# Kernel tuning notes

Hardware: AMD Instinct MI355X
Metric: run time of the kernel (lower is better)

## Reference

```python
import jax, jax.numpy as jnp
import numpy as np

KS = 5
NF = 64
B, H, W = 2, 160, 160


def _conv1x1(x, w, b):
    # x: (B,Ci,H,W), w: (Co,Ci)
    return jnp.einsum('oi,bihw->bohw', w, x) + b[None, :, None, None]


def _conv2x2(x, w, b, dil):
    # x: (B,1,Hp,Wp), w: (64,1,2,2); VALID conv with dilation dil
    y = jax.lax.conv_general_dilated(x, w, (1, 1), 'VALID',
                                     rhs_dilation=(dil, dil),
                                     dimension_numbers=('NCHW', 'OIHW', 'NCHW'))
    return y + b[None, :, None, None]


def _conv_s(x, w, b):
    # conv1 module, mode 's': gather taps (0,0),(1,1),(1,2),(2,1) of each 3x3 patch,
    # then (1,4) conv == linear combo of 4 shifted images.
    h = x.shape[2] - 2
    wd = x.shape[3] - 2
    x0 = x[:, 0]
    taps = jnp.stack([x0[:, 0:h, 0:wd],
                      x0[:, 1:h + 1, 1:wd + 1],
                      x0[:, 1:h + 1, 2:wd + 2],
                      x0[:, 2:h + 2, 1:wd + 1]], axis=1)  # (B,4,h,wd)
    return jnp.einsum('ok,bkhw->bohw', w.reshape(NF, 4), taps) + b[None, :, None, None]


def _construct(c, dense_ps):
    # relu then dense 1x1-conv chain with channel concat, final 1x1 -> 4 channels
    x = jax.nn.relu(c)
    for (wt, bs) in dense_ps[:-1]:
        feat = jax.nn.relu(_conv1x1(x, wt, bs))
        x = jnp.concatenate([x, feat], axis=1)
    wt, bs = dense_ps[-1]
    return _conv1x1(x, wt, bs)


def _ag(x, sigx, sigy, theta, sigr):
    # x: (B,ks,ks,HW); params: (B,HW). Per-pixel anisotropic bilateral kernel.
    ks = x.shape[1]
    r = jnp.arange(ks, dtype=x.dtype) - ks // 2
    sq = (r[:, None] ** 2 + r[None, :] ** 2)[None, :, :, None]  # (1,ks,ks,1)
    sx = sigx[:, None, None, :]
    sy = sigy[:, None, None, :]
    th = theta[:, None, None, :]
    sr = sigr[:, None, None, :]
    spatial = jnp.exp(-sq / (2.0 * sr ** 2))
    disx = jnp.abs(x[:, ks // 2:ks // 2 + 1] - x)       # center row
    disy = jnp.abs(x[:, :, ks // 2:ks // 2 + 1] - x)    # center col
    a = sx * disx
    bb = sy * disy
    color = jnp.exp(-0.5 * (a ** 2 - 2.0 * th * a * bb + bb ** 2))
    kern = spatial * color
    kern = kern / jnp.sum(kern, axis=(1, 2), keepdims=True)
    return jnp.sum(kern * x, axis=(1, 2))  # (B,HW)


def _forward(x_in, conv1x_w, conv1x_b, conv1c_w, conv1c_b, conv1cs_w, conv1cs_b,
             w2, b2, w3, b3, w4, b4, w5, b5, w6, b6):
    dense_ps = [(w2, b2), (w3, b3), (w4, b4), (w5, b5), (w6, b6)]

    def fk(x, mod):
        if mod == 's':
            c = _conv_s(x, conv1cs_w, conv1cs_b)
        elif mod == 'c':
            c = _conv2x2(x, conv1c_w, conv1c_b, 2)
        else:
            c = _conv2x2(x, conv1x_w, conv1x_b, 1)
        return _construct(c, dense_ps)

    def mode_ens(x, p, mod):
        pad = lambda z: jnp.pad(z, ((0, 0), (0, 0), (0, p), (0, p)), mode='reflect')
        r0 = fk(pad(x), mod)
        r2 = jnp.rot90(fk(pad(jnp.rot90(x, 2, (2, 3))), mod), 2, (2, 3))
        r1 = jnp.rot90(fk(pad(jnp.rot90(x, 1, (2, 3))), mod), 3, (2, 3))
        r3 = jnp.rot90(fk(pad(jnp.rot90(x, 3, (2, 3))), mod), 1, (2, 3))
        return (r0 + r2) / 2.0, (r1 + r3) / 2.0

    e1x, e2x = mode_ens(x_in, 1, 'x')
    e1s, e2s = mode_ens(x_in, 2, 's')
    e1c, e2c = mode_ens(x_in, 2, 'c')
    par = (e1x + e2x + e1s + e2s + e1c + e2c) / 6.0  # (B,4,H,W)

    b, c, h, w = x_in.shape
    sigx = jnp.clip(jax.nn.sigmoid(par[:, 0]).reshape(b, -1) + 1e-6, 0.0, 1.0)
    sigy = jnp.clip(jax.nn.sigmoid(par[:, 1]).reshape(b, -1) + 1e-6, 0.0, 1.0)
    theta = jnp.clip(jnp.tanh(par[:, 2]).reshape(b, -1), -1.0, 1.0)
    sigr = jnp.clip(jnp.tanh(par[:, 3]).reshape(b, -1) + 1e-6, -1.0, 1.0)

    ph = KS // 2
    xt = jnp.pad(x_in, ((0, 0), (0, 0), (ph, ph), (ph, ph)))  # zero pad
    # unfold -> (B, KS, KS, H*W)
    patches = jnp.stack([jnp.stack([xt[:, 0, i:i + h, j:j + w].reshape(b, -1)
                                    for j in range(KS)], axis=1)
                         for i in range(KS)], axis=1)
    outs = _ag(patches, sigx * 20.0, sigy * 20.0, theta, sigr * 10.0 + 10.0).reshape(b, c, h, w)
    return outs, sigx, sigy, theta, sigr


def setup_inputs() -> dict:
    key = jax.random.key(0)
    k = jax.random.split(key, 10)
    def kn(kk, shape, fan_in):
        return jax.random.normal(kk, shape, jnp.float32) * np.float32(np.sqrt(2.0 / fan_in))
    zb = lambda n: jnp.zeros((n,), jnp.float32)
    return {
        'x_in': jax.random.normal(k[0], (B, 1, H, W), jnp.float32),
        'conv1x_w': kn(k[1], (NF, 1, 2, 2), 4), 'conv1x_b': zb(NF),
        'conv1c_w': kn(k[2], (NF, 1, 2, 2), 4), 'conv1c_b': zb(NF),
        'conv1cs_w': kn(k[3], (NF, 1, 1, 4), 4), 'conv1cs_b': zb(NF),
        'w2': kn(k[4], (NF, NF), NF), 'b2': zb(NF),
        'w3': kn(k[5], (NF, 2 * NF), 2 * NF), 'b3': zb(NF),
        'w4': kn(k[6], (NF, 3 * NF), 3 * NF), 'b4': zb(NF),
        'w5': kn(k[7], (NF, 4 * NF), 4 * NF), 'b5': zb(NF),
        'w6': kn(k[8], (4, 5 * NF), 5 * NF), 'b6': zb(4),
    }


def reference(x_in, conv1x_w, conv1x_b, conv1c_w, conv1c_b, conv1cs_w, conv1cs_b,
              w2, b2, w3, b3, w4, b4, w5, b5, w6, b6):
    return _forward(x_in, conv1x_w, conv1x_b, conv1c_w, conv1c_b, conv1cs_w, conv1cs_b,
                    w2, b2, w3, b3, w4, b4, w5, b5, w6, b6)
```

## Files before the change

### kernel.cpp

```cpp
#include <hip/hip_runtime.h>
#include <hip/hip_bf16.h>
#include <math.h>
#include <string.h>


#define NN   160
#define NPIX 25600

typedef __attribute__((ext_vector_type(4))) float float4v;
typedef __attribute__((ext_vector_type(8))) unsigned short ushort8;
typedef __attribute__((ext_vector_type(2))) unsigned int uint2v;
typedef __attribute__((ext_vector_type(4))) unsigned int uint4v;
typedef __attribute__((ext_vector_type(8))) __bf16 bf16x8;

__device__ __forceinline__ int refp(int a) { return (a <= NN - 1) ? a : (2 * (NN - 1) - a); }

__device__ __forceinline__ unsigned short f2b(float f) {
    unsigned int x = __float_as_uint(f);
    return (unsigned short)((x + 0x7FFFu + ((x >> 16) & 1u)) >> 16);
}
__device__ __forceinline__ unsigned int pk2(float lo, float hi) {
    float2 f; f.x = lo; f.y = hi;
    __hip_bfloat162 h = __float22bfloat162_rn(f);
    unsigned int u;
    memcpy(&u, &h, 4);
    return u;
}

__global__ __launch_bounds__(256) void bnet_wconv_kernel(
    const float* __restrict__ w2, const float* __restrict__ w3,
    const float* __restrict__ w4, const float* __restrict__ w5,
    const float* __restrict__ w6, unsigned short* __restrict__ wb)
{
    const int t = blockIdx.x * 256 + threadIdx.x;
    if (t < 4096)       wb[t] = f2b(w2[t]);
    else if (t < 12288) wb[t] = f2b(w3[t - 4096]);
    else if (t < 24576) wb[t] = f2b(w4[t - 12288]);
    else if (t < 40960) wb[t] = f2b(w5[t - 24576]);
    else {
        const int i = t - 40960;
        wb[t] = (i < 4 * 320) ? f2b(w6[i]) : (unsigned short)0;
    }
}

template <int NCH>
__device__ __forceinline__ void dense_layer(const ushort8 (&A)[NCH], float4v biasv,
                                            unsigned short* Xs, int w, int lo16, int lq) {
    const int K = NCH * 32;
#pragma unroll
    for (int pp = 0; pp < 2; ++pp) {
        const int px0 = (pp * 2) * 16 + lo16;
        const int px1 = (pp * 2 + 1) * 16 + lo16;
        float4v acc0 = biasv, acc1 = biasv;
#pragma unroll
        for (int s = 0; s < NCH; ++s) {
            const int c8 = s * 4 + lq;
            const bf16x8 bf0 = __builtin_bit_cast(bf16x8, *(const ushort8*)&Xs[c8 * 512 + px0 * 8]);
            const bf16x8 bf1 = __builtin_bit_cast(bf16x8, *(const ushort8*)&Xs[c8 * 512 + px1 * 8]);
            const bf16x8 af  = __builtin_bit_cast(bf16x8, A[s]);
            acc0 = __builtin_amdgcn_mfma_f32_16x16x32_bf16(af, bf0, acc0, 0, 0, 0);
            acc1 = __builtin_amdgcn_mfma_f32_16x16x32_bf16(af, bf1, acc1, 0, 0, 0);
        }
        const int cb = K + w * 16 + lq * 4;
        uint2v o0, o1;
        o0[0] = pk2(fmaxf(acc0[0], 0.0f), fmaxf(acc0[1], 0.0f));
        o0[1] = pk2(fmaxf(acc0[2], 0.0f), fmaxf(acc0[3], 0.0f));
        o1[0] = pk2(fmaxf(acc1[0], 0.0f), fmaxf(acc1[1], 0.0f));
        o1[1] = pk2(fmaxf(acc1[2], 0.0f), fmaxf(acc1[3], 0.0f));
        *(uint2v*)&Xs[(cb >> 3) * 512 + px0 * 8 + (cb & 7)] = o0;
        *(uint2v*)&Xs[(cb >> 3) * 512 + px1 * 8 + (cb & 7)] = o1;
    }
    __syncthreads();
}

__global__ __launch_bounds__(256, 4) void bnet_mlp_kernel(
    const float* __restrict__ x,
    const float* __restrict__ wx, const float* __restrict__ bx,
    const float* __restrict__ wcs, const float* __restrict__ bcs,
    const float* __restrict__ wc, const float* __restrict__ bc,
    const unsigned short* __restrict__ wb,
    const float* __restrict__ b2, const float* __restrict__ b3,
    const float* __restrict__ b4, const float* __restrict__ b5,
    float* __restrict__ par)
{
    __shared__ unsigned short Xs[20480];
    float* red = (float*)Xs;

    const int t = threadIdx.x;
    const int lane = t & 63;
    const int lo16 = lane & 15;
    const int lq = lane >> 4;
    const int w = __builtin_amdgcn_readfirstlane(t >> 6);

    const int bid = blockIdx.x;
    const int tile = bid % 400;
    const int b = (bid / 400) & 1;
    const int mode = (bid / 800) % 3;
    const int k = bid / 2400;

    const float* xb = x + b * NPIX;
    const float* w1 = (mode == 0) ? wx : (mode == 1) ? wcs : wc;
    const float* b1 = (mode == 0) ? bx : (mode == 1) ? bcs : bc;
    int DY[4], DX[4];
    if (mode == 0)      { DY[0]=0; DY[1]=0; DY[2]=1; DY[3]=1;  DX[0]=0; DX[1]=1; DX[2]=0; DX[3]=1; }
    else if (mode == 1) { DY[0]=0; DY[1]=1; DY[2]=1; DY[3]=2;  DX[0]=0; DX[1]=1; DX[2]=2; DX[3]=1; }
    else                { DY[0]=0; DY[1]=0; DY[2]=2; DY[3]=2;  DX[0]=0; DX[1]=2; DX[2]=0; DX[3]=2; }

    const int arow = w * 16 + lo16;
    ushort8 a2[2], a3[4], a4[6], a5[8], a6[3];
#pragma unroll
    for (int s = 0; s < 2; ++s) a2[s] = *(const ushort8*)&wb[arow * 64 + s * 32 + lq * 8];
#pragma unroll
    for (int s = 0; s < 4; ++s) a3[s] = *(const ushort8*)&wb[4096 + arow * 128 + s * 32 + lq * 8];
#pragma unroll
    for (int s = 0; s < 6; ++s) a4[s] = *(const ushort8*)&wb[12288 + arow * 192 + s * 32 + lq * 8];
#pragma unroll
    for (int s = 0; s < 8; ++s) a5[s] = *(const ushort8*)&wb[24576 + arow * 256 + s * 32 + lq * 8];
#pragma unroll
    for (int c = 0; c < 3; ++c) {
        const int ch = (3 * w + c) * 32;
        if (ch < 320) {
            a6[c] = *(const ushort8*)&wb[40960 + lo16 * 320 + ch + lq * 8];
        } else {
            ushort8 z = {0, 0, 0, 0, 0, 0, 0, 0};
            a6[c] = z;
        }
    }
    const float4v b2v = *(const float4v*)&b2[w * 16 + lq * 4];
    const float4v b3v = *(const float4v*)&b3[w * 16 + lq * 4];
    const float4v b4v = *(const float4v*)&b4[w * 16 + lq * 4];
    const float4v b5v = *(const float4v*)&b5[w * 16 + lq * 4];

    const int pix = tile * 64 + lane;
    const int pi = pix / NN;
    const int pj = pix - pi * NN;

    float s4[4];
#pragma unroll
    for (int tt = 0; tt < 4; ++tt) {
        const int dy = DY[tt], dx = DX[tt];
        int r, c;
        if (k == 0)      { r = refp(pi + dy); c = refp(pj + dx); }
        else if (k == 1) { r = refp(pi + dx); c = (pj >= dy) ? (pj - dy) : (dy - pj); }
        else if (k == 2) { r = (pi >= dy) ? (pi - dy) : (dy - pi);
                           c = (pj >= dx) ? (pj - dx) : (dx - pj); }
        else             { r = (pi >= dx) ? (pi - dx) : (dx - pi); c = refp(pj + dy); }
        s4[tt] = xb[r * NN + c];
    }
    float co[16];
#pragma unroll
    for (int oo = 0; oo < 16; ++oo) {
        const int o = w * 16 + oo;
        float cacc = b1[o];
#pragma unroll
        for (int tt = 0; tt < 4; ++tt) cacc = fmaf(w1[o * 4 + tt], s4[tt], cacc);
        co[oo] = fmaxf(cacc, 0.0f);
    }
    uint4v pka, pkb;
#pragma unroll
    for (int q = 0; q < 4; ++q) {
        pka[q] = pk2(co[2 * q], co[2 * q + 1]);
        pkb[q] = pk2(co[8 + 2 * q], co[9 + 2 * q]);
    }
    *(uint4v*)&Xs[(w * 2) * 512 + lane * 8]     = pka;
    *(uint4v*)&Xs[(w * 2 + 1) * 512 + lane * 8] = pkb;
    __syncthreads();

    dense_layer<2>(a2, b2v, Xs, w, lo16, lq);
    dense_layer<4>(a3, b3v, Xs, w, lo16, lq);
    dense_layer<6>(a4, b4v, Xs, w, lo16, lq);
    dense_layer<8>(a5, b5v, Xs, w, lo16, lq);

    float4v acc6[4];
#pragma unroll
    for (int pt = 0; pt < 4; ++pt) { float4v z = {0.f, 0.f, 0.f, 0.f}; acc6[pt] = z; }
#pragma unroll
    for (int pt = 0; pt < 4; ++pt) {
        const int px = pt * 16 + lo16;
#pragma unroll
        for (int c = 0; c < 3; ++c) {
            int chb = (3 * w + c) * 32;
            chb = (chb < 288) ? chb : 288;
            const int c8 = (chb >> 3) + lq;
            const bf16x8 bf = __builtin_bit_cast(
                bf16x8, *(const ushort8*)&Xs[c8 * 512 + px * 8]);
            const bf16x8 af = __builtin_bit_cast(bf16x8, a6[c]);
            acc6[pt] = __builtin_amdgcn_mfma_f32_16x16x32_bf16(af, bf, acc6[pt], 0, 0, 0);
        }
    }
    __syncthreads();

    if (lq == 0) {
#pragma unroll
        for (int pt = 0; pt < 4; ++pt)
            *(float4v*)&red[(((w * 4) + pt) * 16 + lo16) * 4] = acc6[pt];
    }
    __syncthreads();
    if (w == 0) {
        float4v sv;
#pragma unroll
        for (int r = 0; r < 4; ++r)
            sv[r] = red[(((0 * 4) + lq) * 16 + lo16) * 4 + r]
                  + red[(((1 * 4) + lq) * 16 + lo16) * 4 + r]
                  + red[(((2 * 4) + lq) * 16 + lo16) * 4 + r]
                  + red[(((3 * 4) + lq) * 16 + lo16) * 4 + r];
        const int pixg = tile * 64 + lq * 16 + lo16;
#pragma unroll
        for (int r = 0; r < 4; ++r)
            atomicAdd(&par[(r * 2 + b) * NPIX + pixg], sv[r]);
    }
}

__global__ __launch_bounds__(256) void bnet_bilateral_kernel(
    const float* __restrict__ x, const float* __restrict__ b6,
    float* __restrict__ out)
{
    const int tid = blockIdx.x * 256 + threadIdx.x;
    const int b = tid / NPIX;
    const int pix = tid - b * NPIX;
    const int pi = pix / NN;
    const int pj = pix - pi * NN;

    float* par = out + 2 * NPIX;
    const float inv12 = 1.0f / 12.0f;
    const float p0 = par[(0 + b) * NPIX + pix] * inv12 + b6[0];
    const float p1 = par[(2 + b) * NPIX + pix] * inv12 + b6[1];
    const float p2 = par[(4 + b) * NPIX + pix] * inv12 + b6[2];
    const float p3 = par[(6 + b) * NPIX + pix] * inv12 + b6[3];

    float sigx = 1.0f / (1.0f + __expf(-p0)) + 1e-6f;
    sigx = fminf(fmaxf(sigx, 0.0f), 1.0f);
    float sigy = 1.0f / (1.0f + __expf(-p1)) + 1e-6f;
    sigy = fminf(fmaxf(sigy, 0.0f), 1.0f);
    float t2 = __expf(2.0f * fminf(fmaxf(p2, -15.0f), 15.0f));
    float th = (t2 - 1.0f) / (t2 + 1.0f);
    th = fminf(fmaxf(th, -1.0f), 1.0f);
    float t3 = __expf(2.0f * fminf(fmaxf(p3, -15.0f), 15.0f));
    float sigr = (t3 - 1.0f) / (t3 + 1.0f) + 1e-6f;
    sigr = fminf(fmaxf(sigr, -1.0f), 1.0f);

    par[(0 + b) * NPIX + pix] = sigx;
    par[(2 + b) * NPIX + pix] = sigy;
    par[(4 + b) * NPIX + pix] = th;
    par[(6 + b) * NPIX + pix] = sigr;

    const float sx = sigx * 20.0f;
    const float sy = sigy * 20.0f;
    const float sr = sigr * 10.0f + 10.0f;

    const float* xb = x + b * NPIX;
    float patch[5][5];
#pragma unroll
    for (int ky = 0; ky < 5; ++ky) {
#pragma unroll
        for (int kx = 0; kx < 5; ++kx) {
            const int r = pi + ky - 2, c = pj + kx - 2;
            patch[ky][kx] = (r >= 0 && r < NN && c >= 0 && c < NN) ? xb[r * NN + c] : 0.0f;
        }
    }

    const float inv2sr2 = 1.0f / (2.0f * sr * sr);
    float num = 0.0f, den = 0.0f;
#pragma unroll
    for (int ky = 0; ky < 5; ++ky) {
#pragma unroll
        for (int kx = 0; kx < 5; ++kx) {
            const float v = patch[ky][kx];
            const float dxv = fabsf(patch[2][kx] - v);
            const float dyv = fabsf(patch[ky][2] - v);
            const float a = sx * dxv;
            const float bb = sy * dyv;
            const float sq = (float)((ky - 2) * (ky - 2) + (kx - 2) * (kx - 2));
            const float kern = __expf(-sq * inv2sr2 - 0.5f * (a * a - 2.0f * th * a * bb + bb * bb));
            den += kern;
            num = fmaf(kern, v, num);
        }
    }
    out[tid] = num / den;
}

extern "C" void kernel_launch(void* const* d_in, const int* in_sizes, int n_in,
                              void* d_out, int out_size, void* d_ws, size_t ws_size,
                              hipStream_t stream) {
    const float* x   = (const float*)d_in[0];
    const float* wx  = (const float*)d_in[1];
    const float* bx  = (const float*)d_in[2];
    const float* wc  = (const float*)d_in[3];
    const float* bc  = (const float*)d_in[4];
    const float* wcs = (const float*)d_in[5];
    const float* bcs = (const float*)d_in[6];
    const float* w2  = (const float*)d_in[7];
    const float* b2  = (const float*)d_in[8];
    const float* w3  = (const float*)d_in[9];
    const float* b3  = (const float*)d_in[10];
    const float* w4  = (const float*)d_in[11];
    const float* b4  = (const float*)d_in[12];
    const float* w5  = (const float*)d_in[13];
    const float* b5  = (const float*)d_in[14];
    const float* w6  = (const float*)d_in[15];
    const float* b6  = (const float*)d_in[16];
    float* out = (float*)d_out;
    unsigned short* wb = (unsigned short*)d_ws;

    (void)hipMemsetAsync(out + 2 * NPIX, 0, 8 * NPIX * sizeof(float), stream);

    hipLaunchKernelGGL(bnet_wconv_kernel, dim3(180), dim3(256), 0, stream,
                       w2, w3, w4, w5, w6, wb);

    hipLaunchKernelGGL(bnet_mlp_kernel, dim3(9600), dim3(256), 0, stream,
                       x, wx, bx, wcs, bcs, wc, bc,
                       wb, b2, b3, b4, b5,
                       out + 2 * NPIX);

    hipLaunchKernelGGL(bnet_bilateral_kernel, dim3(200), dim3(256), 0, stream,
                       x, b6, out);
}
```

Baseline: 198.9 us.

## Make MLP kernel persistent and convert weights to bf16 in-kernel

The MLP kernel becomes a persistent grid of 768 blocks, each looping over 12-13 (tile, batch, mode, k) work items. Each block loads its MFMA weight fragments into registers once, converting fp32 to bf16 on the fly. This removes the separate weight-conversion kernel launch and the per-block weight reload that 9600 short-lived blocks paid. In exchange, occupancy is capped at 3 blocks per CU and an extra barrier is added per iteration.

```diff
diff --git a/kernel.cpp b/kernel.cpp
--- a/kernel.cpp
+++ b/kernel.cpp
@@ -15,10 +15,6 @@
 
 __device__ __forceinline__ int refp(int a) { return (a <= NN - 1) ? a : (2 * (NN - 1) - a); }
 
-__device__ __forceinline__ unsigned short f2b(float f) {
-    unsigned int x = __float_as_uint(f);
-    return (unsigned short)((x + 0x7FFFu + ((x >> 16) & 1u)) >> 16);
-}
 __device__ __forceinline__ unsigned int pk2(float lo, float hi) {
     float2 f; f.x = lo; f.y = hi;
     __hip_bfloat162 h = __float22bfloat162_rn(f);
@@ -26,21 +22,13 @@
     memcpy(&u, &h, 4);
     return u;
 }
-
-__global__ __launch_bounds__(256) void bnet_wconv_kernel(
-    const float* __restrict__ w2, const float* __restrict__ w3,
-    const float* __restrict__ w4, const float* __restrict__ w5,
-    const float* __restrict__ w6, unsigned short* __restrict__ wb)
-{
-    const int t = blockIdx.x * 256 + threadIdx.x;
-    if (t < 4096)       wb[t] = f2b(w2[t]);
-    else if (t < 12288) wb[t] = f2b(w3[t - 4096]);
-    else if (t < 24576) wb[t] = f2b(w4[t - 12288]);
-    else if (t < 40960) wb[t] = f2b(w5[t - 24576]);
-    else {
-        const int i = t - 40960;
-        wb[t] = (i < 4 * 320) ? f2b(w6[i]) : (unsigned short)0;
-    }
+__device__ __forceinline__ ushort8 cvt8(const float* __restrict__ p) {
+    const float4v f0 = *(const float4v*)p;
+    const float4v f1 = *(const float4v*)(p + 4);
+    uint4v u;
+    u[0] = pk2(f0[0], f0[1]); u[1] = pk2(f0[2], f0[3]);
+    u[2] = pk2(f1[0], f1[1]); u[3] = pk2(f1[2], f1[3]);
+    return __builtin_bit_cast(ushort8, u);
 }
 
 template <int NCH>
@@ -73,14 +61,16 @@
     __syncthreads();
 }
 
-__global__ __launch_bounds__(256, 4) void bnet_mlp_kernel(
+__global__ __launch_bounds__(256, 3) void bnet_mlp_kernel(
     const float* __restrict__ x,
     const float* __restrict__ wx, const float* __restrict__ bx,
     const float* __restrict__ wcs, const float* __restrict__ bcs,
     const float* __restrict__ wc, const float* __restrict__ bc,
-    const unsigned short* __restrict__ wb,
-    const float* __restrict__ b2, const float* __restrict__ b3,
-    const float* __restrict__ b4, const float* __restrict__ b5,
+    const float* __restrict__ w2, const float* __restrict__ b2,
+    const float* __restrict__ w3, const float* __restrict__ b3,
+    const float* __restrict__ w4, const float* __restrict__ b4,
+    const float* __restrict__ w5, const float* __restrict__ b5,
+    const float* __restrict__ w6,
     float* __restrict__ par)
 {
     __shared__ unsigned short Xs[20480];
@@ -92,35 +82,21 @@
     const int lq = lane >> 4;
     const int w = __builtin_amdgcn_readfirstlane(t >> 6);
 
-    const int bid = blockIdx.x;
-    const int tile = bid % 400;
-    const int b = (bid / 400) & 1;
-    const int mode = (bid / 800) % 3;
-    const int k = bid / 2400;
-
-    const float* xb = x + b * NPIX;
-    const float* w1 = (mode == 0) ? wx : (mode == 1) ? wcs : wc;
-    const float* b1 = (mode == 0) ? bx : (mode == 1) ? bcs : bc;
-    int DY[4], DX[4];
-    if (mode == 0)      { DY[0]=0; DY[1]=0; DY[2]=1; DY[3]=1;  DX[0]=0; DX[1]=1; DX[2]=0; DX[3]=1; }
-    else if (mode == 1) { DY[0]=0; DY[1]=1; DY[2]=1; DY[3]=2;  DX[0]=0; DX[1]=1; DX[2]=2; DX[3]=1; }
-    else                { DY[0]=0; DY[1]=0; DY[2]=2; DY[3]=2;  DX[0]=0; DX[1]=2; DX[2]=0; DX[3]=2; }
-
     const int arow = w * 16 + lo16;
     ushort8 a2[2], a3[4], a4[6], a5[8], a6[3];
 #pragma unroll
-    for (int s = 0; s < 2; ++s) a2[s] = *(const ushort8*)&wb[arow * 64 + s * 32 + lq * 8];
-#pragma unroll
-    for (int s = 0; s < 4; ++s) a3[s] = *(const ushort8*)&wb[4096 + arow * 128 + s * 32 + lq * 8];
-#pragma unroll
-    for (int s = 0; s < 6; ++s) a4[s] = *(const ushort8*)&wb[12288 + arow * 192 + s * 32 + lq * 8];
-#pragma unroll
-    for (int s = 0; s < 8; ++s) a5[s] = *(const ushort8*)&wb[24576 + arow * 256 + s * 32 + lq * 8];
+    for (int s = 0; s < 2; ++s) a2[s] = cvt8(&w2[arow * 64 + s * 32 + lq * 8]);
+#pragma unroll
+    for (int s = 0; s < 4; ++s) a3[s] = cvt8(&w3[arow * 128 + s * 32 + lq * 8]);
+#pragma unroll
+    for (int s = 0; s < 6; ++s) a4[s] = cvt8(&w4[arow * 192 + s * 32 + lq * 8]);
+#pragma unroll
+    for (int s = 0; s < 8; ++s) a5[s] = cvt8(&w5[arow * 256 + s * 32 + lq * 8]);
 #pragma unroll
     for (int c = 0; c < 3; ++c) {
         const int ch = (3 * w + c) * 32;
-        if (ch < 320) {
-            a6[c] = *(const ushort8*)&wb[40960 + lo16 * 320 + ch + lq * 8];
+        if (ch < 320 && lo16 < 4) {
+            a6[c] = cvt8(&w6[lo16 * 320 + ch + lq * 8]);
         } else {
             ushort8 z = {0, 0, 0, 0, 0, 0, 0, 0};
             a6[c] = z;
@@ -131,83 +107,107 @@
     const float4v b4v = *(const float4v*)&b4[w * 16 + lq * 4];
     const float4v b5v = *(const float4v*)&b5[w * 16 + lq * 4];
 
-    const int pix = tile * 64 + lane;
-    const int pi = pix / NN;
-    const int pj = pix - pi * NN;
-
-    float s4[4];
-#pragma unroll
-    for (int tt = 0; tt < 4; ++tt) {
-        const int dy = DY[tt], dx = DX[tt];
-        int r, c;
-        if (k == 0)      { r = refp(pi + dy); c = refp(pj + dx); }
-        else if (k == 1) { r = refp(pi + dx); c = (pj >= dy) ? (pj - dy) : (dy - pj); }
-        else if (k == 2) { r = (pi >= dy) ? (pi - dy) : (dy - pi);
-                           c = (pj >= dx) ? (pj - dx) : (dx - pj); }
-        else             { r = (pi >= dx) ? (pi - dx) : (dx - pi); c = refp(pj + dy); }
-        s4[tt] = xb[r * NN + c];
-    }
-    float co[16];
-#pragma unroll
-    for (int oo = 0; oo < 16; ++oo) {
-        const int o = w * 16 + oo;
-        float cacc = b1[o];
-#pragma unroll
-        for (int tt = 0; tt < 4; ++tt) cacc = fmaf(w1[o * 4 + tt], s4[tt], cacc);
-        co[oo] = fmaxf(cacc, 0.0f);
-    }
-    uint4v pka, pkb;
-#pragma unroll
-    for (int q = 0; q < 4; ++q) {
-        pka[q] = pk2(co[2 * q], co[2 * q + 1]);
-        pkb[q] = pk2(co[8 + 2 * q], co[9 + 2 * q]);
-    }
-    *(uint4v*)&Xs[(w * 2) * 512 + lane * 8]     = pka;
-    *(uint4v*)&Xs[(w * 2 + 1) * 512 + lane * 8] = pkb;
-    __syncthreads();
-
-    dense_layer<2>(a2, b2v, Xs, w, lo16, lq);
-    dense_layer<4>(a3, b3v, Xs, w, lo16, lq);
-    dense_layer<6>(a4, b4v, Xs, w, lo16, lq);
-    dense_layer<8>(a5, b5v, Xs, w, lo16, lq);
-
-    float4v acc6[4];
-#pragma unroll
-    for (int pt = 0; pt < 4; ++pt) { float4v z = {0.f, 0.f, 0.f, 0.f}; acc6[pt] = z; }
-#pragma unroll
-    for (int pt = 0; pt < 4; ++pt) {
-        const int px = pt * 16 + lo16;
-#pragma unroll
-        for (int c = 0; c < 3; ++c) {
-            int chb = (3 * w + c) * 32;
-            chb = (chb < 288) ? chb : 288;
-            const int c8 = (chb >> 3) + lq;
-            const bf16x8 bf = __builtin_bit_cast(
-                bf16x8, *(const ushort8*)&Xs[c8 * 512 + px * 8]);
-            const bf16x8 af = __builtin_bit_cast(bf16x8, a6[c]);
-            acc6[pt] = __builtin_amdgcn_mfma_f32_16x16x32_bf16(af, bf, acc6[pt], 0, 0, 0);
-        }
-    }
-    __syncthreads();
-
-    if (lq == 0) {
-#pragma unroll
-        for (int pt = 0; pt < 4; ++pt)
-            *(float4v*)&red[(((w * 4) + pt) * 16 + lo16) * 4] = acc6[pt];
-    }
-    __syncthreads();
-    if (w == 0) {
-        float4v sv;
-#pragma unroll
-        for (int r = 0; r < 4; ++r)
-            sv[r] = red[(((0 * 4) + lq) * 16 + lo16) * 4 + r]
-                  + red[(((1 * 4) + lq) * 16 + lo16) * 4 + r]
-                  + red[(((2 * 4) + lq) * 16 + lo16) * 4 + r]
-                  + red[(((3 * 4) + lq) * 16 + lo16) * 4 + r];
-        const int pixg = tile * 64 + lq * 16 + lo16;
-#pragma unroll
-        for (int r = 0; r < 4; ++r)
-            atomicAdd(&par[(r * 2 + b) * NPIX + pixg], sv[r]);
+    const int bid = blockIdx.x;
+    const int nit = 12 + (bid < 384 ? 1 : 0);
+    const int g0  = (bid < 384) ? bid * 13 : bid * 12 + 384;
+
+    for (int it = 0; it < nit; ++it) {
+        const int g = g0 + it;
+        const int v = g % 12;
+        const int tb = g / 12;
+        const int tile = tb >> 1;
+        const int b = tb & 1;
+        const int mode = v >> 2;
+        const int k = v & 3;
+
+        const float* xb = x + b * NPIX;
+        const float* w1 = (mode == 0) ? wx : (mode == 1) ? wcs : wc;
+        const float* b1 = (mode == 0) ? bx : (mode == 1) ? bcs : bc;
+        int DY[4], DX[4];
+        if (mode == 0)      { DY[0]=0; DY[1]=0; DY[2]=1; DY[3]=1;  DX[0]=0; DX[1]=1; DX[2]=0; DX[3]=1; }
+        else if (mode == 1) { DY[0]=0; DY[1]=1; DY[2]=1; DY[3]=2;  DX[0]=0; DX[1]=1; DX[2]=2; DX[3]=1; }
+        else                { DY[0]=0; DY[1]=0; DY[2]=2; DY[3]=2;  DX[0]=0; DX[1]=2; DX[2]=0; DX[3]=2; }
+
+        const int pix = tile * 64 + lane;
+        const int pi = pix / NN;
+        const int pj = pix - pi * NN;
+
+        __syncthreads();
+
+        float s4[4];
+#pragma unroll
+        for (int tt = 0; tt < 4; ++tt) {
+            const int dy = DY[tt], dx = DX[tt];
+            int r, c;
+            if (k == 0)      { r = refp(pi + dy); c = refp(pj + dx); }
+            else if (k == 1) { r = refp(pi + dx); c = (pj >= dy) ? (pj - dy) : (dy - pj); }
+            else if (k == 2) { r = (pi >= dy) ? (pi - dy) : (dy - pi);
+                               c = (pj >= dx) ? (pj - dx) : (dx - pj); }
+            else             { r = (pi >= dx) ? (pi - dx) : (dx - pi); c = refp(pj + dy); }
+            s4[tt] = xb[r * NN + c];
+        }
+        float co[16];
+#pragma unroll
+        for (int oo = 0; oo < 16; ++oo) {
+            const int o = w * 16 + oo;
+            float cacc = b1[o];
+#pragma unroll
+            for (int tt = 0; tt < 4; ++tt) cacc = fmaf(w1[o * 4 + tt], s4[tt], cacc);
+            co[oo] = fmaxf(cacc, 0.0f);
+        }
+        uint4v pka, pkb;
+#pragma unroll
+        for (int q = 0; q < 4; ++q) {
+            pka[q] = pk2(co[2 * q], co[2 * q + 1]);
+            pkb[q] = pk2(co[8 + 2 * q], co[9 + 2 * q]);
+        }
+        *(uint4v*)&Xs[(w * 2) * 512 + lane * 8]     = pka;
+        *(uint4v*)&Xs[(w * 2 + 1) * 512 + lane * 8] = pkb;
+        __syncthreads();
+
+        dense_layer<2>(a2, b2v, Xs, w, lo16, lq);
+        dense_layer<4>(a3, b3v, Xs, w, lo16, lq);
+        dense_layer<6>(a4, b4v, Xs, w, lo16, lq);
+        dense_layer<8>(a5, b5v, Xs, w, lo16, lq);
+
+        float4v acc6[4];
+#pragma unroll
+        for (int pt = 0; pt < 4; ++pt) { float4v z = {0.f, 0.f, 0.f, 0.f}; acc6[pt] = z; }
+#pragma unroll
+        for (int pt = 0; pt < 4; ++pt) {
+            const int px = pt * 16 + lo16;
+#pragma unroll
+            for (int c = 0; c < 3; ++c) {
+                int chb = (3 * w + c) * 32;
+                chb = (chb < 288) ? chb : 288;
+                const int c8 = (chb >> 3) + lq;
+                const bf16x8 bf = __builtin_bit_cast(
+                    bf16x8, *(const ushort8*)&Xs[c8 * 512 + px * 8]);
+                const bf16x8 af = __builtin_bit_cast(bf16x8, a6[c]);
+                acc6[pt] = __builtin_amdgcn_mfma_f32_16x16x32_bf16(af, bf, acc6[pt], 0, 0, 0);
+            }
+        }
+        __syncthreads();
+
+        if (lq == 0) {
+#pragma unroll
+            for (int pt = 0; pt < 4; ++pt)
+                *(float4v*)&red[(((w * 4) + pt) * 16 + lo16) * 4] = acc6[pt];
+        }
+        __syncthreads();
+        if (w == 0) {
+            float4v sv;
+#pragma unroll
+            for (int r = 0; r < 4; ++r)
+                sv[r] = red[(((0 * 4) + lq) * 16 + lo16) * 4 + r]
+                      + red[(((1 * 4) + lq) * 16 + lo16) * 4 + r]
+                      + red[(((2 * 4) + lq) * 16 + lo16) * 4 + r]
+                      + red[(((3 * 4) + lq) * 16 + lo16) * 4 + r];
+            const int pixg = tile * 64 + lq * 16 + lo16;
+#pragma unroll
+            for (int r = 0; r < 4; ++r)
+                atomicAdd(&par[(r * 2 + b) * NPIX + pixg], sv[r]);
+        }
     }
 }
 
@@ -300,16 +300,12 @@
     const float* w6  = (const float*)d_in[15];
     const float* b6  = (const float*)d_in[16];
     float* out = (float*)d_out;
-    unsigned short* wb = (unsigned short*)d_ws;
 
     (void)hipMemsetAsync(out + 2 * NPIX, 0, 8 * NPIX * sizeof(float), stream);
 
-    hipLaunchKernelGGL(bnet_wconv_kernel, dim3(180), dim3(256), 0, stream,
-                       w2, w3, w4, w5, w6, wb);
-
-    hipLaunchKernelGGL(bnet_mlp_kernel, dim3(9600), dim3(256), 0, stream,
+    hipLaunchKernelGGL(bnet_mlp_kernel, dim3(768), dim3(256), 0, stream,
                        x, wx, bx, wcs, bcs, wc, bc,
-                       wb, b2, b3, b4, b5,
+                       w2, b2, w3, b3, w4, b4, w5, b5, w6,
                        out + 2 * NPIX);
 
     hipLaunchKernelGGL(bnet_bilateral_kernel, dim3(200), dim3(256), 0, stream,
```

New measurement: 182.9 us. 1.09x faster.
